# Kernel optimization log

Measured on AMD Instinct MI355X. Metric: run time of the kernel, lower is better.

Reference implementation:

```python
import jax, jax.numpy as jnp
import numpy as np

K = 8
EPS = 1e-5

def knn_idx(x, k):
    # x: (B, C, N) -> idx (B, N, k) nearest neighbors (incl. self)
    xt = jnp.swapaxes(x, 1, 2)  # (B, N, C)
    inner = -2.0 * jnp.einsum('bnc,bmc->bnm', xt, xt)
    xx = jnp.sum(xt * xt, axis=-1)  # (B, N)
    neg_dist = -xx[:, :, None] - inner - xx[:, None, :]
    return jax.lax.top_k(neg_dist, k)[1]

def graph_feature(x, k):
    # x: (B, C, N) -> (B, 2C, N, k)
    B, C, N = x.shape
    idx = knn_idx(x, k)  # (B, N, k)
    xt = jnp.swapaxes(x, 1, 2)  # (B, N, C)
    nb = xt[jnp.arange(B)[:, None, None], idx]  # (B, N, k, C)
    center = xt[:, :, None, :]
    feat = jnp.concatenate([nb - center, jnp.broadcast_to(center, nb.shape)], axis=-1)
    return jnp.transpose(feat, (0, 3, 1, 2))

def bn2d(h, g, b):
    m = jnp.mean(h, axis=(0, 2, 3), keepdims=True)
    v = jnp.var(h, axis=(0, 2, 3), keepdims=True)
    return g[None, :, None, None] * (h - m) * jax.lax.rsqrt(v + EPS) + b[None, :, None, None]

def bn1d(h, g, b):
    m = jnp.mean(h, axis=(0, 2), keepdims=True)
    v = jnp.var(h, axis=(0, 2), keepdims=True)
    return g[None, :, None] * (h - m) * jax.lax.rsqrt(v + EPS) + b[None, :, None]

def fps_idx(xyz, m):
    # xyz: (B, N, 3) furthest point sampling starting at index 0 -> (B, m) int32
    B, N, _ = xyz.shape
    def body(carry, _):
        dist, last = carry
        lastp = jnp.take_along_axis(xyz, last[:, None, None], axis=1)  # (B,1,3)
        d = jnp.sum((xyz - lastp) ** 2, axis=-1)
        dist = jnp.minimum(dist, d)
        nxt = jnp.argmax(dist, axis=-1).astype(jnp.int32)
        return (dist, nxt), last
    init = (jnp.full((B, N), 1e10, dtype=xyz.dtype), jnp.zeros((B,), jnp.int32))
    _, idxs = jax.lax.scan(body, init, None, length=m)
    return jnp.swapaxes(idxs, 0, 1)  # (B, m)

def fps_downsample(coor, x, m):
    # coor: (B,3,N), x: (B,C,N)
    idx = fps_idx(jnp.swapaxes(coor, 1, 2), m)  # (B, m)
    B = coor.shape[0]
    comb = jnp.concatenate([coor, x], axis=1)  # (B, 3+C, N)
    g = jnp.take_along_axis(comb, idx[:, None, :], axis=2)
    return g[:, :3], g[:, 3:]

def edge_block(h, w, g, b):
    f = graph_feature(h, K)                      # (B, 2C, N, k)
    f = jnp.einsum('oc,bcnk->bonk', w, f)        # 1x1 conv2d, no bias
    f = jax.nn.leaky_relu(bn2d(f, g, b), 0.2)
    return jnp.max(f, axis=-1)                   # (B, O, N)

def setup_inputs() -> dict:
    key = jax.random.key(0)
    ks = jax.random.split(key, 16)
    H = 2048
    c16, c8, c4, c2 = H // 16, H // 8, H // 4, H // 2  # 128,256,512,1024
    O2 = 4096 // 2  # 2048
    def w(k, o, c):
        return jax.random.normal(k, (o, c), jnp.float32) * (1.0 / np.sqrt(c))
    inp = {
        'x': jax.random.normal(ks[0], (8, 3, 2048), jnp.float32),
        'w1': w(ks[1], c16, 6),
        'w2': w(ks[2], c16, c8),
        'w3': w(ks[3], c8, c8),
        'w4': w(ks[4], c4, c4),
        'w5': w(ks[5], O2, c2),
        'rw1': w(ks[6], c16, c16),
        'rw2': w(ks[7], c8, c16),
        'rw3': w(ks[8], c4, c8),
    }
    for i, (nm, ch) in enumerate([('1', c16), ('2', c16), ('3', c8), ('4', c4), ('5', O2)]):
        kk = jax.random.split(ks[9 + i], 2)
        inp['g' + nm] = 1.0 + 0.1 * jax.random.normal(kk[0], (ch,), jnp.float32)
        inp['b' + nm] = 0.1 * jax.random.normal(kk[1], (ch,), jnp.float32)
    return inp

def reference(x, w1, w2, w3, w4, w5, rw1, rw2, rw3, g1, b1, g2, b2, g3, b3, g4, b4, g5, b5):
    coor = x
    x1 = edge_block(x, w1, g1, b1)
    x2 = edge_block(x1, w2, g2, b2) + jnp.einsum('oc,bcn->bon', rw1, x1)
    x3 = edge_block(x2, w3, g3, b3) + jnp.einsum('oc,bcn->bon', rw2, x2)
    x4 = edge_block(x3, w4, g4, b4) + jnp.einsum('oc,bcn->bon', rw3, x3)
    h = jnp.concatenate([x1, x2, x3, x4], axis=1)  # (B, 1024, N)
    h = jax.nn.leaky_relu(bn1d(jnp.einsum('oc,bcn->bon', w5, h), g5, b5), 0.2)
    for m in (512, 256, 128):
        coor, h = fps_downsample(coor, h, m)
    f = jnp.concatenate([jnp.max(h, axis=-1), jnp.mean(h, axis=-1)], axis=1)  # (B, 4096)
    return coor, f
```

## Files before the change

### kernel.cpp

```cpp
#include <hip/hip_runtime.h>
#include <float.h>

#define NPTS 2048
#define NB 8
#define KNN 8

typedef short bf16x8 __attribute__((ext_vector_type(8)));
typedef float f32x4  __attribute__((ext_vector_type(4)));

__device__ __forceinline__ float leakyf(float x){ return x > 0.f ? x : 0.2f*x; }

__device__ __forceinline__ unsigned short f2bf(float f){
    unsigned u = __float_as_uint(f);
    return (unsigned short)((u + 0x7FFF + ((u>>16)&1)) >> 16);
}

#define BET(v1,i1,v2,i2) (((v1)>(v2)) || ((v1)==(v2) && (i1)<(i2)))

__device__ __forceinline__ void ins8(float tv[8], int tix[8], float v, int ci)
{
    if (BET(v,ci,tv[7],tix[7])){
        tv[7]=v; tix[7]=ci;
#pragma unroll
        for (int q=7;q>=1;q--){
            if (BET(tv[q],tix[q],tv[q-1],tix[q-1])){
                float t=tv[q]; tv[q]=tv[q-1]; tv[q-1]=t;
                int ti=tix[q]; tix[q]=tix[q-1]; tix[q-1]=ti;
            }
        }
    }
}

__device__ __forceinline__ void merge_write8(float tv[8], int tix[8], int lane,
                                             int* __restrict__ dst)
{
#pragma unroll
    for (int r=0;r<8;r++){
        float bv = tv[0]; int bi = tix[0];
#pragma unroll
        for (int off=32; off; off>>=1){
            float ov = __shfl_xor(bv, off); int oi = __shfl_xor(bi, off);
            if (BET(ov,oi,bv,bi)){ bv=ov; bi=oi; }
        }
        if (tv[0]==bv && tix[0]==bi){
#pragma unroll
            for (int q=0;q<7;q++){ tv[q]=tv[q+1]; tix[q]=tix[q+1]; }
            tv[7]=-FLT_MAX; tix[7]=0x7fffffff;
        }
        if (lane==0) dst[r] = bi;
    }
}

__global__ void transpose_x(const float* __restrict__ x, float* __restrict__ xt)
{
    int g = blockIdx.x*256 + threadIdx.x;
    if (g >= NB*NPTS) return;
    int b = g >> 11, n = g & 2047;
    const float* xb = x + (long)b*3*NPTS;
    xt[g*3+0] = xb[n];
    xt[g*3+1] = xb[NPTS+n];
    xt[g*3+2] = xb[2*NPTS+n];
}

__device__ __forceinline__ unsigned long long u64max(unsigned long long a,
                                                     unsigned long long b)
{ return a > b ? a : b; }

template<int CTRL>
__device__ __forceinline__ unsigned long long dpp_max_step(unsigned long long v)
{
    unsigned plo = (unsigned)__builtin_amdgcn_update_dpp(0, (int)(unsigned)v,      CTRL, 0xF, 0xF, true);
    unsigned phi = (unsigned)__builtin_amdgcn_update_dpp(0, (int)(unsigned)(v>>32), CTRL, 0xF, 0xF, true);
    unsigned long long p = ((unsigned long long)phi << 32) | plo;
    return u64max(v, p);
}

__device__ __forceinline__ unsigned long long wave_reduce_max(unsigned long long v)
{
    v = dpp_max_step<0x111>(v);
    v = dpp_max_step<0x112>(v);
    v = dpp_max_step<0x114>(v);
    v = dpp_max_step<0x118>(v);
    v = dpp_max_step<0x142>(v);
    v = dpp_max_step<0x143>(v);
    return v;
}

template<int NPP>
__device__ void fps_stage_mw(const float4* __restrict__ pts, int m, int* sel,
                             int tid, unsigned long long* wv)
{
    float cx[NPP], cy[NPP], cz[NPP], dist[NPP];
#pragma unroll
    for (int r=0;r<NPP;r++){
        float4 p = pts[r*256 + tid];
        cx[r]=p.x; cy[r]=p.y; cz[r]=p.z; dist[r]=1e10f;
    }
    int w = tid>>6, lane = tid&63;
    int last = 0;
    if (tid==0) sel[0]=0;
    for (int i=1;i<m;i++){
        float4 lp = pts[last];
#pragma unroll
        for (int r=0;r<NPP;r++){
            float dx=__fsub_rn(cx[r],lp.x), dy=__fsub_rn(cy[r],lp.y), dz=__fsub_rn(cz[r],lp.z);
            float d = __fadd_rn(__fadd_rn(__fmul_rn(dx,dx), __fmul_rn(dy,dy)), __fmul_rn(dz,dz));
            dist[r] = fminf(dist[r], d);
        }
        unsigned long long t[(NPP+1)/2];
        if (NPP == 1){
            t[0] = ((unsigned long long)__float_as_uint(dist[0])<<32) | (unsigned)(2047 - tid);
        } else {
#pragma unroll
            for (int k=0;k<NPP/2;k++){
                unsigned long long a = ((unsigned long long)__float_as_uint(dist[2*k  ])<<32) | (unsigned)(2047 - ((2*k  )*256+tid));
                unsigned long long b = ((unsigned long long)__float_as_uint(dist[2*k+1])<<32) | (unsigned)(2047 - ((2*k+1)*256+tid));
                t[k] = u64max(a, b);
            }
#pragma unroll
            for (int s=NPP/4; s>=1; s>>=1)
#pragma unroll
                for (int k=0;k<s;k++) t[k] = u64max(t[k], t[k+s]);
        }
        unsigned long long best = wave_reduce_max(t[0]);
        if (lane==63) wv[(i&1)*4 + w] = best;
        __syncthreads();
        unsigned long long b0 = wv[(i&1)*4+0], b1 = wv[(i&1)*4+1];
        unsigned long long b2 = wv[(i&1)*4+2], b3 = wv[(i&1)*4+3];
        best = u64max(u64max(b0,b1), u64max(b2,b3));
        int win = 2047 - (int)(unsigned)best;
        last = win;
        if (tid==0) sel[i] = win;
    }
}

struct FpsSh {
    float4 pts1[2048]; float4 pts2[512]; float4 pts3[256];
    int sel1[512]; int sel2[256]; int sel3[128];
    unsigned long long wv[8];
};
struct GemmSh { __align__(16) float As[16][132]; __align__(16) float Bs[16][132]; };
union ShU { FpsSh f; GemmSh g; };

__device__ void fps_block(const float* __restrict__ x, int* __restrict__ idxF,
                          float* __restrict__ coorOut, int b, int tid, FpsSh& sh)
{
    const float* xb = x + (long)b*3*NPTS;
    for (int i=tid;i<2048;i+=256)
        sh.pts1[i] = make_float4(xb[i], xb[NPTS+i], xb[2*NPTS+i], 0.f);
    __syncthreads();
    fps_stage_mw<8>(sh.pts1, 512, sh.sel1, tid, sh.wv);
    __syncthreads();
    for (int i=tid;i<512;i+=256) sh.pts2[i] = sh.pts1[sh.sel1[i]];
    __syncthreads();
    fps_stage_mw<2>(sh.pts2, 256, sh.sel2, tid, sh.wv);
    __syncthreads();
    for (int i=tid;i<256;i+=256) sh.pts3[i] = sh.pts2[sh.sel2[i]];
    __syncthreads();
    fps_stage_mw<1>(sh.pts3, 128, sh.sel3, tid, sh.wv);
    __syncthreads();
    for (int i=tid;i<128;i+=256){
        int gi = sh.sel1[sh.sel2[sh.sel3[i]]];
        idxF[b*128+i] = gi;
        float4 p = sh.pts1[gi];
        coorOut[(long)b*384 + 0*128 + i] = p.x;
        coorOut[(long)b*384 + 1*128 + i] = p.y;
        coorOut[(long)b*384 + 2*128 + i] = p.z;
    }
}

__global__ __launch_bounds__(256)
void knn_c3(const float* __restrict__ x, int* __restrict__ idx)
{
    __shared__ float sx[NPTS], sy[NPTS], sz[NPTS];
    int b = blockIdx.x >> 7, rblk = blockIdx.x & 127;
    const float* xb = x + (long)b*3*NPTS;
    int tid = threadIdx.x;
    for (int i=tid;i<NPTS;i+=256){
        sx[i]=xb[i]; sy[i]=xb[NPTS+i]; sz[i]=xb[2*NPTS+i];
    }
    __syncthreads();
    int w = tid>>6, lane = tid&63;
    for (int rr=0; rr<4; rr++){
        int n = rblk*16 + w*4 + rr;
        float px=sx[n], py=sy[n], pz=sz[n];
        float tv[8]; int tix[8];
#pragma unroll
        for (int i=0;i<8;i++){ tv[i]=-FLT_MAX; tix[i]=0x7fffffff; }
        for (int it=0; it<8; it++){
            int c = it*256 + lane*4;
            float4 qx = *(const float4*)&sx[c];
            float4 qy = *(const float4*)&sy[c];
            float4 qz = *(const float4*)&sz[c];
            float dx, dy, dz;
            dx=qx.x-px; dy=qy.x-py; dz=qz.x-pz;
            ins8(tv,tix, -fmaf(dx,dx,fmaf(dy,dy,dz*dz)), c+0);
            dx=qx.y-px; dy=qy.y-py; dz=qz.y-pz;
            ins8(tv,tix, -fmaf(dx,dx,fmaf(dy,dy,dz*dz)), c+1);
            dx=qx.z-px; dy=qy.z-py; dz=qz.z-pz;
            ins8(tv,tix, -fmaf(dx,dx,fmaf(dy,dy,dz*dz)), c+2);
            dx=qx.w-px; dy=qy.w-py; dz=qz.w-pz;
            ins8(tv,tix, -fmaf(dx,dx,fmaf(dy,dy,dz*dz)), c+3);
        }
        merge_write8(tv, tix, lane, idx + ((long)(b*NPTS+n))*KNN);
    }
}

__global__ void prep_w(const float* __restrict__ w, const float* __restrict__ rw,
                       float* __restrict__ wcat, int O, int C, int hasR)
{
    int t = blockIdx.x*256 + threadIdx.x;
    if (t >= O*C) return;
    int o = t / C, c = t % C;
    float a = w[o*2*C + c];
    wcat[o*C + c] = a;
    wcat[(O+o)*C + c] = w[o*2*C + C + c] - a;
    if (hasR) wcat[(2*O+o)*C + c] = rw[o*C + c];
}

__global__ void rownorm(const float* __restrict__ X, float* __restrict__ xx,
                        int lda, int C)
{
    int g = blockIdx.x*256 + threadIdx.x;
    if (g >= NB*NPTS) return;
    const float* r = X + (long)g*lda;
    float s = 0.f;
    for (int c=0;c<C;c++) s += r[c]*r[c];
    xx[g] = s;
}

template<int VEC, bool SYM>
__device__ __forceinline__ void gemm_body(
    float (*As)[132], float (*Bs)[132],
    const float* __restrict__ A, const float* __restrict__ B, float* __restrict__ C,
    int Kd, int lda, int ldb, int ldc, int bx, int by, int tid)
{
    int tm = by * 128, tn = bx * 128;
    int ty = tid >> 4, tx = tid & 15;
    int cn0 = tx*4, cn1 = 64 + tx*4;
    float acc[8][8] = {};
    for (int k0 = 0; k0 < Kd; k0 += 16){
        if (VEC == 4){
#pragma unroll
            for (int i=0;i<2;i++){
                int e = tid + i*256;
                int rr = e >> 2, kq = e & 3;
                float4 av = *(const float4*)(A + (long)(tm+rr)*lda + k0 + kq*4);
                float4 bv = *(const float4*)(B + (long)(tn+rr)*ldb + k0 + kq*4);
                As[kq*4+0][rr]=av.x; As[kq*4+1][rr]=av.y; As[kq*4+2][rr]=av.z; As[kq*4+3][rr]=av.w;
                Bs[kq*4+0][rr]=bv.x; Bs[kq*4+1][rr]=bv.y; Bs[kq*4+2][rr]=bv.z; Bs[kq*4+3][rr]=bv.w;
            }
        } else {
#pragma unroll
            for (int i=0;i<8;i++){
                int e = tid + i*256;
                int kk = e & 15, rr = e >> 4;
                int ak = k0 + kk;
                As[kk][rr] = (ak < Kd) ? A[(long)(tm+rr)*lda + ak] : 0.f;
                Bs[kk][rr] = (ak < Kd) ? B[(long)(tn+rr)*ldb + ak] : 0.f;
            }
        }
        __syncthreads();
#pragma unroll
        for (int kk=0;kk<16;kk++){
            float4 a01 = *(const float4*)&As[kk][ty*8];
            float4 a23 = *(const float4*)&As[kk][ty*8+4];
            float4 b01 = *(const float4*)&Bs[kk][cn0];
            float4 b23 = *(const float4*)&Bs[kk][cn1];
            float aa[8] = {a01.x,a01.y,a01.z,a01.w,a23.x,a23.y,a23.z,a23.w};
            float bb[8] = {b01.x,b01.y,b01.z,b01.w,b23.x,b23.y,b23.z,b23.w};
#pragma unroll
            for (int i=0;i<8;i++)
#pragma unroll
                for (int j=0;j<8;j++)
                    acc[i][j] += aa[i]*bb[j];
        }
        __syncthreads();
    }
#pragma unroll
    for (int i=0;i<8;i++){
        long r = tm + ty*8 + i;
        float4 v0 = {acc[i][0],acc[i][1],acc[i][2],acc[i][3]};
        float4 v1 = {acc[i][4],acc[i][5],acc[i][6],acc[i][7]};
        *(float4*)(C + r*ldc + tn + cn0) = v0;
        *(float4*)(C + r*ldc + tn + cn1) = v1;
    }
    if (SYM && bx != by){
#pragma unroll
        for (int j=0;j<4;j++){
            long r0 = tn + cn0 + j;
            long r1 = tn + cn1 + j;
            float4 u0 = {acc[0][j],  acc[1][j],  acc[2][j],  acc[3][j]};
            float4 u1 = {acc[4][j],  acc[5][j],  acc[6][j],  acc[7][j]};
            float4 u2 = {acc[0][j+4],acc[1][j+4],acc[2][j+4],acc[3][j+4]};
            float4 u3 = {acc[4][j+4],acc[5][j+4],acc[6][j+4],acc[7][j+4]};
            *(float4*)(C + r0*ldc + tm + ty*8)     = u0;
            *(float4*)(C + r0*ldc + tm + ty*8 + 4) = u1;
            *(float4*)(C + r1*ldc + tm + ty*8)     = u2;
            *(float4*)(C + r1*ldc + tm + ty*8 + 4) = u3;
        }
    }
}

template<int VEC, bool SYM>
__global__ __launch_bounds__(256)
void gemm_nt(const float* __restrict__ A, const float* __restrict__ B,
             float* __restrict__ C,
             int Kd, int lda, int ldb, int ldc,
             long sA, long sB, long sC)
{
    if (SYM && blockIdx.y > blockIdx.x) return;
    __shared__ GemmSh sh;
    int bz = blockIdx.z;
    gemm_body<VEC,SYM>(sh.As, sh.Bs, A + (long)bz*sA, B + (long)bz*sB,
                       C + (long)bz*sC, Kd, lda, ldb, ldc,
                       blockIdx.x, blockIdx.y, threadIdx.x);
}

__global__ __launch_bounds__(256)
void uvr_fps(const float* __restrict__ A, const float* __restrict__ B,
             float* __restrict__ C, int Kd, int lda, int ldb, int ldc, int nx,
             const float* __restrict__ x, int* __restrict__ idxF,
             float* __restrict__ coorOut)
{
    __shared__ ShU sh;
    if (blockIdx.x < 8){
        fps_block(x, idxF, coorOut, blockIdx.x, threadIdx.x, sh.f);
        return;
    }
    int id = blockIdx.x - 8;
    gemm_body<4,false>(sh.g.As, sh.g.Bs, A, B, C, Kd, lda, ldb, ldc,
                       id % nx, id / nx, threadIdx.x);
}

__global__ __launch_bounds__(256)
void topk8(const float* __restrict__ D, const float* __restrict__ xx,
           int* __restrict__ idx, int b0)
{
    int tid = threadIdx.x, w = tid>>6, lane = tid & 63;
    int gr = blockIdx.x*4 + w;
    int b = b0 + (gr >> 11);
    const float* drow = D + (long)gr*NPTS;
    const float* xb = xx + (long)b*NPTS;
    float tv[8]; int tix[8];
#pragma unroll
    for (int i=0;i<8;i++){ tv[i]=-FLT_MAX; tix[i]=0x7fffffff; }
    for (int it=0; it<8; it++){
        int c = it*256 + lane*4;
        float4 d4 = *(const float4*)(drow + c);
        float4 x4 = *(const float4*)(xb + c);
        ins8(tv,tix, 2.f*d4.x - x4.x, c+0);
        ins8(tv,tix, 2.f*d4.y - x4.y, c+1);
        ins8(tv,tix, 2.f*d4.z - x4.z, c+2);
        ins8(tv,tix, 2.f*d4.w - x4.w, c+3);
    }
    merge_write8(tv, tix, lane, idx + ((long)(b0*NPTS) + gr)*KNN);
}

__global__ __launch_bounds__(256)
void stats_edge(const float* __restrict__ uvr, const int* __restrict__ idx,
                float* __restrict__ ps, float* __restrict__ pq,
                float* __restrict__ mxb, float* __restrict__ mnb,
                int O, int ld)
{
    int tid = threadIdx.x;
    int r0 = blockIdx.x * 128;
    float s0=0,q0=0,s1=0,q1=0;
    for (int rr=0; rr<128; rr++){
        int g = r0 + rr;
        int b = g >> 11;
        const int* ip = idx + (long)g*KNN;
        const float* vrow = uvr + (long)g*ld + O;
        const float* ub[8];
#pragma unroll
        for (int k=0;k<8;k++) ub[k] = uvr + (long)((b<<11) + ip[k])*ld;
        int o = tid;
        if (o < O){
            float vv = vrow[o];
            float mx=-FLT_MAX, mn=FLT_MAX;
#pragma unroll
            for (int k=0;k<8;k++){
                float f = ub[k][o]+vv;
                s0+=f; q0+=f*f; mx=fmaxf(mx,f); mn=fminf(mn,f);
            }
            mxb[(long)g*O+o]=mx; mnb[(long)g*O+o]=mn;
        }
        o = tid + 256;
        if (o < O){
            float vv = vrow[o];
            float mx=-FLT_MAX, mn=FLT_MAX;
#pragma unroll
            for (int k=0;k<8;k++){
                float f = ub[k][o]+vv;
                s1+=f; q1+=f*f; mx=fmaxf(mx,f); mn=fminf(mn,f);
            }
            mxb[(long)g*O+o]=mx; mnb[(long)g*O+o]=mn;
        }
    }
    if (tid < O){ ps[blockIdx.x*2048 + tid] = s0; pq[blockIdx.x*2048 + tid] = q0; }
    if (tid+256 < O){ ps[blockIdx.x*2048 + tid+256] = s1; pq[blockIdx.x*2048 + tid+256] = q1; }
}

__global__ void reduce_stats(const float* __restrict__ ps, const float* __restrict__ pq,
                             const float* __restrict__ gam, const float* __restrict__ bet,
                             float* __restrict__ ab, float* __restrict__ cb,
                             int O, int np, float invCnt)
{
    int o = blockIdx.x*256 + threadIdx.x;
    if (o >= O) return;
    float s=0.f, q=0.f;
    for (int p=0;p<np;p++){ s += ps[p*2048 + o]; q += pq[p*2048 + o]; }
    float m = s * invCnt;
    float var = q * invCnt - m*m;
    float a = gam[o] * rsqrtf(var + 1e-5f);
    ab[o] = a;
    cb[o] = bet[o] - m*a;
}

__global__ void finalize_edge(const float* __restrict__ mxb, const float* __restrict__ mnb,
                              const float* __restrict__ uvr,
                              const float* __restrict__ ab, const float* __restrict__ cb,
                              float* __restrict__ hcat, int lgO, int ld, int hoff, int hasR)
{
    long t = (long)blockIdx.x*256 + threadIdx.x;
    int O = 1 << lgO;
    int o = (int)(t & (O-1));
    int g = (int)(t >> lgO);
    float a = ab[o], c = cb[o];
    float mx = mxb[t], mn = mnb[t];
    float zz = (a > 0.f) ? (a*mx + c) : (a*mn + c);
    float outv = leakyf(zz);
    if (hasR) outv += uvr[(long)g*ld + 2*O + o];
    hcat[(long)g*1024 + hoff + o] = outv;
}

__global__ void colsum_fin(const float* __restrict__ part, float* __restrict__ hbar)
{
    int tid = threadIdx.x;
    float4 acc = {0,0,0,0};
    for (int p=0;p<128;p++){
        float4 v = ((const float4*)part)[p*256 + tid];
        acc.x+=v.x; acc.y+=v.y; acc.z+=v.z; acc.w+=v.w;
    }
    ((float4*)hbar)[tid] = acc;
}

__global__ __launch_bounds__(256)
void gram_colsum(const float* __restrict__ H, float* __restrict__ P,
                 float* __restrict__ cspart)
{
    __shared__ __align__(16) unsigned short As[128][40];
    __shared__ __align__(16) unsigned short Bs[128][40];
    int tid = threadIdx.x;
    if (blockIdx.x >= 288){
        int pb = blockIdx.x - 288;
        const float4* h4 = (const float4*)(H + (long)pb*128*1024);
        float4 acc = {0,0,0,0};
        for (int r=0;r<128;r++){
            float4 v = h4[r*256 + tid];
            acc.x+=v.x; acc.y+=v.y; acc.z+=v.z; acc.w+=v.w;
        }
        ((float4*)cspart)[pb*256 + tid] = acc;
        return;
    }
    int bz = blockIdx.x / 36, t36 = blockIdx.x % 36;
    int I = 0, q = t36, accq = 8;
    while (q >= accq){ q -= accq; accq--; I++; }
    int ti = (I + q)*128, tj = I*128;
    int w = tid>>6, lane = tid&63;
    int wr = (w>>1)*64, wc = (w&1)*64;
    f32x4 acc[16];
#pragma unroll
    for (int i=0;i<16;i++) acc[i] = (f32x4){0.f,0.f,0.f,0.f};
    const float* Hc = H + (long)bz*2048*1024;
    for (int m0=0; m0<2048; m0+=32){
#pragma unroll
        for (int it=0; it<4; it++){
            int e = tid + it*256;
            int mm = e >> 5;
            int c4 = (e & 31) * 4;
            const float* row = Hc + (long)(m0+mm)*1024;
            float4 av = *(const float4*)(row + ti + c4);
            float4 bv = *(const float4*)(row + tj + c4);
            int mg = mm >> 3, ml = mm & 7;
            float fa[4] = {av.x, av.y, av.z, av.w};
            float fb[4] = {bv.x, bv.y, bv.z, bv.w};
#pragma unroll
            for (int qq=0; qq<4; qq++){
                int ia = c4 + qq;
                int pos = ((mg ^ ((ia>>2)&3))<<3) + ml;
                As[ia][pos] = f2bf(fa[qq]);
                Bs[ia][pos] = f2bf(fb[qq]);
            }
        }
        __syncthreads();
        bf16x8 af[4], bf[4];
#pragma unroll
        for (int f=0; f<4; f++){
            int ra = wr + f*16 + (lane&15);
            int ga = ((lane>>4) ^ ((ra>>2)&3)) << 3;
            af[f] = *(const bf16x8*)&As[ra][ga];
            int rb = wc + f*16 + (lane&15);
            int gb = ((lane>>4) ^ ((rb>>2)&3)) << 3;
            bf[f] = *(const bf16x8*)&Bs[rb][gb];
        }
#pragma unroll
        for (int fi=0; fi<4; fi++)
#pragma unroll
        for (int fj=0; fj<4; fj++)
            acc[fi*4+fj] = __builtin_amdgcn_mfma_f32_16x16x32_bf16(
                af[fi], bf[fj], acc[fi*4+fj], 0, 0, 0);
        __syncthreads();
    }
    float* Pp = P + ((long)bz<<20);
#pragma unroll
    for (int fi=0; fi<4; fi++)
#pragma unroll
    for (int fj=0; fj<4; fj++){
        int row0 = ti + wr + fi*16 + (lane>>4)*4;
        int col  = tj + wc + fj*16 + (lane&15);
#pragma unroll
        for (int r4=0; r4<4; r4++)
            Pp[(long)(row0+r4)*1024 + col] = acc[fi*4+fj][r4];
    }
}

__global__ void greduce(const float* __restrict__ P, float* __restrict__ G)
{
    long i4 = (long)blockIdx.x*256 + threadIdx.x;
    float4 a = ((const float4*)P)[i4];
    for (int p=1;p<8;p++){
        float4 v = ((const float4*)P)[((long)p<<18) + i4];
        a.x+=v.x; a.y+=v.y; a.z+=v.z; a.w+=v.w;
    }
    ((float4*)G)[i4] = a;
}

__global__ void mirror_g(float* __restrict__ G)
{
    __shared__ float t[64][65];
    int q = blockIdx.x, I = 0, acc = 15;
    while (q >= acc){ q -= acc; acc--; I++; }
    int J = I + 1 + q;
    int tid = threadIdx.x;
#pragma unroll
    for (int k=0;k<16;k++){
        int e = tid + k*256;
        int sr = e>>6, sc = e&63;
        t[sr][sc] = G[(long)(J*64+sr)*1024 + I*64+sc];
    }
    __syncthreads();
#pragma unroll
    for (int k=0;k<16;k++){
        int e = tid + k*256;
        int dr = e>>6, dc = e&63;
        G[(long)(I*64+dr)*1024 + J*64+dc] = t[dc][dr];
    }
}

__global__ void bn5_prep(const float* __restrict__ w5, const float* __restrict__ T,
                         const float* __restrict__ hbar,
                         const float* __restrict__ g5, const float* __restrict__ b5,
                         float* __restrict__ ab, float* __restrict__ cb)
{
    int w = threadIdx.x>>6, lane = threadIdx.x&63;
    int n = blockIdx.x*4 + w;
    const float4* wr = (const float4*)(w5 + (long)n*1024);
    const float4* tr = (const float4*)(T  + (long)n*1024);
    const float4* hb = (const float4*)hbar;
    float s1=0.f, s2=0.f;
    for (int i=lane;i<256;i+=64){
        float4 wv = wr[i], t4 = tr[i], hv = hb[i];
        s1 += wv.x*hv.x + wv.y*hv.y + wv.z*hv.z + wv.w*hv.w;
        s2 += wv.x*t4.x + wv.y*t4.y + wv.z*t4.z + wv.w*t4.w;
    }
#pragma unroll
    for (int off=32; off; off>>=1){
        s1 += __shfl_xor(s1, off);
        s2 += __shfl_xor(s2, off);
    }
    if (lane==0){
        float m = s1*(1.f/16384.f);
        float qq = s2*(1.f/16384.f);
        float var = qq - m*m;
        float a = g5[n]*rsqrtf(var+1e-5f);
        ab[n]=a; cb[n]=b5[n]-m*a;
    }
}

__global__ void gather_rows(const float* __restrict__ src, const int* __restrict__ idxF,
                            float* __restrict__ dst)
{
    int r = blockIdx.x;
    int b = r >> 7;
    int srow = (b<<11) + idxF[r];
    const float4* s = (const float4*)(src + (long)srow*1024);
    float4* d = (float4*)(dst + (long)r*1024);
    for (int c=threadIdx.x; c<256; c+=256) d[c] = s[c];
}

__global__ void finalize_f(const float* __restrict__ zsel, const float* __restrict__ ab,
                           const float* __restrict__ cb, float* __restrict__ out)
{
    int b = blockIdx.x >> 3, oc = blockIdx.x & 7;
    int o = oc*256 + threadIdx.x;
    float a = ab[o], c = cb[o];
    float mx = -FLT_MAX, sm = 0.f;
    const float* zp = zsel + (long)b*128*2048 + o;
    for (int i=0;i<128;i++){
        float v = leakyf(a*zp[(long)i*2048] + c);
        mx = fmaxf(mx, v); sm += v;
    }
    out[b*4096 + o] = mx;
    out[b*4096 + 2048 + o] = sm * (1.f/128.f);
}

extern "C" void kernel_launch(void* const* d_in, const int* in_sizes, int n_in,
                              void* d_out, int out_size, void* d_ws, size_t ws_size,
                              hipStream_t stream)
{
    (void)in_sizes; (void)n_in; (void)out_size; (void)ws_size;
    const float* x   = (const float*)d_in[0];
    const float* w1  = (const float*)d_in[1];
    const float* w2  = (const float*)d_in[2];
    const float* w3  = (const float*)d_in[3];
    const float* w4  = (const float*)d_in[4];
    const float* w5  = (const float*)d_in[5];
    const float* rw1 = (const float*)d_in[6];
    const float* rw2 = (const float*)d_in[7];
    const float* rw3 = (const float*)d_in[8];
    const float* g1  = (const float*)d_in[9];  const float* b1 = (const float*)d_in[10];
    const float* g2  = (const float*)d_in[11]; const float* b2 = (const float*)d_in[12];
    const float* g3  = (const float*)d_in[13]; const float* b3 = (const float*)d_in[14];
    const float* g4  = (const float*)d_in[15]; const float* b4 = (const float*)d_in[16];
    const float* g5  = (const float*)d_in[17]; const float* b5 = (const float*)d_in[18];
    float* out = (float*)d_out;

    char* wsb = (char*)d_ws;
    size_t off = 0;
    auto alloc = [&](size_t bytes)->char* {
        char* p = wsb + off;
        off += (bytes + 255) & ~(size_t)255;
        return p;
    };
    float* xt    = (float*)alloc((size_t)16384*3*4);
    float* hcat  = (float*)alloc((size_t)16384*1024*4);
    float* uvr   = (float*)alloc((size_t)16384*1536*4);
    float* Dbuf  = uvr;
    float* gramP = uvr;
    float* G     = (float*)alloc((size_t)1024*1024*4);
    float* T     = (float*)alloc((size_t)2048*1024*4);
    float* zselA = (float*)alloc((size_t)1024*1024*4);
    float* zsel  = (float*)alloc((size_t)1024*2048*4);
    float* mxb   = (float*)alloc((size_t)16384*512*4);
    float* mnb   = (float*)alloc((size_t)16384*512*4);
    float* xx    = (float*)alloc((size_t)16384*4);
    int*   idx   = (int*)  alloc((size_t)16384*8*4);
    float* wcat  = (float*)alloc((size_t)1536*256*4);
    float* ps    = (float*)alloc((size_t)128*2048*4);
    float* pq    = (float*)alloc((size_t)128*2048*4);
    float* cspart= (float*)alloc((size_t)128*1024*4);
    float* hbar  = (float*)alloc((size_t)1024*4);
    float* ab    = (float*)alloc((size_t)2048*4);
    float* cb    = (float*)alloc((size_t)2048*4);
    int*   idxF  = (int*)  alloc((size_t)1024*4);

    transpose_x<<<64, 256, 0, stream>>>(x, xt);

    struct EB {
        const float* X; int lda, C, O, lgO, hoff, hasR;
        const float* w; const float* rw; const float* g; const float* bb;
    };
    EB eb[4] = {
        { xt,        3,    3,   128, 7, 0,   0, w1, nullptr, g1, b1 },
        { hcat+0,    1024, 128, 128, 7, 128, 1, w2, rw1,     g2, b2 },
        { hcat+128,  1024, 128, 256, 8, 256, 1, w3, rw2,     g3, b3 },
        { hcat+256,  1024, 256, 512, 9, 512, 1, w4, rw3,     g4, b4 },
    };
    for (int i=0;i<4;i++){
        EB e = eb[i];
        int ld = (2 + e.hasR) * e.O;
        int nx = ld / 128;
        int tot = e.O * e.C;
        prep_w<<<(tot+255)/256, 256, 0, stream>>>(e.w, e.rw, wcat, e.O, e.C, e.hasR);
        if (i == 0){
            knn_c3<<<1024, 256, 0, stream>>>(x, idx);
            gemm_nt<1,false><<<dim3(nx, 128, 1), 256, 0, stream>>>(
                e.X, wcat, uvr, e.C, e.lda, e.C, ld, 0, 0, 0);
        } else {
            rownorm<<<64, 256, 0, stream>>>(e.X, xx, e.lda, e.C);
            for (int b0=0; b0<8; b0+=4){
                const float* Ab = e.X + (long)b0*NPTS*e.lda;
                gemm_nt<4,true><<<dim3(16,16,4), 256, 0, stream>>>(
                    Ab, Ab, Dbuf, e.C, e.lda, e.lda, 2048,
                    (long)NPTS*e.lda, (long)NPTS*e.lda, (long)NPTS*NPTS);
                topk8<<<2048, 256, 0, stream>>>(Dbuf, xx, idx, b0);
            }
            if (i == 3)
                uvr_fps<<<8 + nx*128, 256, 0, stream>>>(
                    e.X, wcat, uvr, e.C, e.lda, e.C, ld, nx, x, idxF, out);
            else
                gemm_nt<4,false><<<dim3(nx, 128, 1), 256, 0, stream>>>(
                    e.X, wcat, uvr, e.C, e.lda, e.C, ld, 0, 0, 0);
        }
        stats_edge<<<128, 256, 0, stream>>>(uvr, idx, ps, pq, mxb, mnb, e.O, ld);
        reduce_stats<<<(e.O+255)/256, 256, 0, stream>>>(ps, pq, e.g, e.bb, ab, cb,
                                                        e.O, 128, 1.f/131072.f);
        finalize_edge<<<64*e.O, 256, 0, stream>>>(mxb, mnb, uvr, ab, cb, hcat,
                                                  e.lgO, ld, e.hoff, e.hasR);
    }

    gram_colsum<<<288 + 128, 256, 0, stream>>>(hcat, gramP, cspart);
    colsum_fin<<<1, 256, 0, stream>>>(cspart, hbar);
    greduce<<<1024, 256, 0, stream>>>(gramP, G);
    mirror_g<<<120, 256, 0, stream>>>(G);
    gemm_nt<4,false><<<dim3(8,16,1), 256, 0, stream>>>(
        w5, G, T, 1024, 1024, 1024, 1024, 0, 0, 0);
    bn5_prep<<<512, 256, 0, stream>>>(w5, T, hbar, g5, b5, ab, cb);
    gather_rows<<<1024, 256, 0, stream>>>(hcat, idxF, zselA);
    gemm_nt<4,false><<<dim3(16,8,1), 256, 0, stream>>>(
        zselA, w5, zsel, 1024, 1024, 1024, 2048, 0, 0, 0);
    finalize_f<<<64, 256, 0, stream>>>(zsel, ab, cb, out + 3072);
}
```

Baseline: 3.052 ms.

## Merge kNN Gram and edge GEMM into one launch; split-K small tail GEMMs

For edge blocks 2-4, a single launch now runs the symmetric Gram GEMM for the first four batches alongside the edge-feature GEMM (and FPS for the last block). This fills the GPU better and removes one serialized launch. Dbuf grows to hold four batches and is reused for the mxb/mnb buffers. The two late 1024-K GEMMs (w5·G and zsel) are split four ways along K into partial buffers that bn5_prep and finalize_f sum, which exposes more blocks on small grids at the cost of extra partial-sum traffic and tighter buffer aliasing.

```diff
diff --git a/kernel.cpp b/kernel.cpp
--- a/kernel.cpp
+++ b/kernel.cpp
@@ -141,6 +141,11 @@
 };
 struct GemmSh { __align__(16) float As[16][132]; __align__(16) float Bs[16][132]; };
 union ShU { FpsSh f; GemmSh g; };
+
+template<bool B> struct ShPick { using T = GemmSh; };
+template<> struct ShPick<true> { using T = ShU; };
+__device__ __forceinline__ GemmSh& gemsh(GemmSh& s){ return s; }
+__device__ __forceinline__ GemmSh& gemsh(ShU& u){ return u.g; }
 
 __device__ void fps_block(const float* __restrict__ x, int* __restrict__ idxF,
                           float* __restrict__ coorOut, int b, int tid, FpsSh& sh)
@@ -317,20 +322,32 @@
                        blockIdx.x, blockIdx.y, threadIdx.x);
 }
 
+template<bool FPS>
 __global__ __launch_bounds__(256)
-void uvr_fps(const float* __restrict__ A, const float* __restrict__ B,
-             float* __restrict__ C, int Kd, int lda, int ldb, int ldc, int nx,
-             const float* __restrict__ x, int* __restrict__ idxF,
-             float* __restrict__ coorOut)
-{
-    __shared__ ShU sh;
-    if (blockIdx.x < 8){
-        fps_block(x, idxF, coorOut, blockIdx.x, threadIdx.x, sh.f);
+void edge_mega(const float* __restrict__ X, const float* __restrict__ W,
+               float* __restrict__ D, float* __restrict__ U,
+               int Kd, int lda, int ld, int nxU,
+               const float* __restrict__ x, int* __restrict__ idxF,
+               float* __restrict__ coorOut)
+{
+    __shared__ typename ShPick<FPS>::T sh;
+    int id = blockIdx.x;
+    if constexpr (FPS){
+        if (id < 8){ fps_block(x, idxF, coorOut, id, threadIdx.x, ((ShU&)sh).f); return; }
+        id -= 8;
+    }
+    GemmSh& g = gemsh(sh);
+    if (id < 1024){
+        int bz = id >> 8, r = id & 255, by = r >> 4, bx = r & 15;
+        if (by > bx) return;
+        const float* Xz = X + (long)bz*NPTS*lda;
+        gemm_body<4,true>(g.As, g.Bs, Xz, Xz, D + (long)bz*NPTS*NPTS,
+                          Kd, lda, lda, 2048, bx, by, threadIdx.x);
         return;
     }
-    int id = blockIdx.x - 8;
-    gemm_body<4,false>(sh.g.As, sh.g.Bs, A, B, C, Kd, lda, ldb, ldc,
-                       id % nx, id / nx, threadIdx.x);
+    id -= 1024;
+    gemm_body<4,false>(g.As, g.Bs, X, W, U, Kd, lda, Kd, ld,
+                       id % nxU, id / nxU, threadIdx.x);
 }
 
 __global__ __launch_bounds__(256)
@@ -566,11 +583,17 @@
     int w = threadIdx.x>>6, lane = threadIdx.x&63;
     int n = blockIdx.x*4 + w;
     const float4* wr = (const float4*)(w5 + (long)n*1024);
-    const float4* tr = (const float4*)(T  + (long)n*1024);
+    const float4* t0 = (const float4*)(T + (long)n*1024);
+    const float4* t1 = (const float4*)(T + (1L<<21) + (long)n*1024);
+    const float4* t2 = (const float4*)(T + (2L<<21) + (long)n*1024);
+    const float4* t3 = (const float4*)(T + (3L<<21) + (long)n*1024);
     const float4* hb = (const float4*)hbar;
     float s1=0.f, s2=0.f;
     for (int i=lane;i<256;i+=64){
-        float4 wv = wr[i], t4 = tr[i], hv = hb[i];
+        float4 wv = wr[i], hv = hb[i];
+        float4 a0=t0[i], a1=t1[i], a2=t2[i], a3=t3[i];
+        float4 t4 = {a0.x+a1.x+a2.x+a3.x, a0.y+a1.y+a2.y+a3.y,
+                     a0.z+a1.z+a2.z+a3.z, a0.w+a1.w+a2.w+a3.w};
         s1 += wv.x*hv.x + wv.y*hv.y + wv.z*hv.z + wv.w*hv.w;
         s2 += wv.x*t4.x + wv.y*t4.y + wv.z*t4.z + wv.w*t4.w;
     }
@@ -607,8 +630,11 @@
     float a = ab[o], c = cb[o];
     float mx = -FLT_MAX, sm = 0.f;
     const float* zp = zsel + (long)b*128*2048 + o;
+    const long PS = (long)1024*2048;
     for (int i=0;i<128;i++){
-        float v = leakyf(a*zp[(long)i*2048] + c);
+        long ofs = (long)i*2048;
+        float z = zp[ofs] + zp[PS+ofs] + zp[2*PS+ofs] + zp[3*PS+ofs];
+        float v = leakyf(a*z + c);
         mx = fmaxf(mx, v); sm += v;
     }
     out[b*4096 + o] = mx;
@@ -646,14 +672,14 @@
     float* xt    = (float*)alloc((size_t)16384*3*4);
     float* hcat  = (float*)alloc((size_t)16384*1024*4);
     float* uvr   = (float*)alloc((size_t)16384*1536*4);
-    float* Dbuf  = uvr;
     float* gramP = uvr;
+    float* T     = uvr;
+    float* zsel  = uvr + (size_t)8*1024*1024;
+    float* Dbuf  = (float*)alloc((size_t)4*2048*2048*4);
+    float* mxb   = Dbuf;
+    float* mnb   = Dbuf + (size_t)16384*512;
     float* G     = (float*)alloc((size_t)1024*1024*4);
-    float* T     = (float*)alloc((size_t)2048*1024*4);
     float* zselA = (float*)alloc((size_t)1024*1024*4);
-    float* zsel  = (float*)alloc((size_t)1024*2048*4);
-    float* mxb   = (float*)alloc((size_t)16384*512*4);
-    float* mnb   = (float*)alloc((size_t)16384*512*4);
     float* xx    = (float*)alloc((size_t)16384*4);
     int*   idx   = (int*)  alloc((size_t)16384*8*4);
     float* wcat  = (float*)alloc((size_t)1536*256*4);
@@ -680,28 +706,28 @@
     for (int i=0;i<4;i++){
         EB e = eb[i];
         int ld = (2 + e.hasR) * e.O;
-        int nx = ld / 128;
+        int nxU = ld / 128;
         int tot = e.O * e.C;
         prep_w<<<(tot+255)/256, 256, 0, stream>>>(e.w, e.rw, wcat, e.O, e.C, e.hasR);
         if (i == 0){
             knn_c3<<<1024, 256, 0, stream>>>(x, idx);
-            gemm_nt<1,false><<<dim3(nx, 128, 1), 256, 0, stream>>>(
+            gemm_nt<1,false><<<dim3(nxU, 128, 1), 256, 0, stream>>>(
                 e.X, wcat, uvr, e.C, e.lda, e.C, ld, 0, 0, 0);
         } else {
             rownorm<<<64, 256, 0, stream>>>(e.X, xx, e.lda, e.C);
-            for (int b0=0; b0<8; b0+=4){
-                const float* Ab = e.X + (long)b0*NPTS*e.lda;
-                gemm_nt<4,true><<<dim3(16,16,4), 256, 0, stream>>>(
-                    Ab, Ab, Dbuf, e.C, e.lda, e.lda, 2048,
-                    (long)NPTS*e.lda, (long)NPTS*e.lda, (long)NPTS*NPTS);
-                topk8<<<2048, 256, 0, stream>>>(Dbuf, xx, idx, b0);
-            }
             if (i == 3)
-                uvr_fps<<<8 + nx*128, 256, 0, stream>>>(
-                    e.X, wcat, uvr, e.C, e.lda, e.C, ld, nx, x, idxF, out);
+                edge_mega<true><<<8 + 1024 + nxU*128, 256, 0, stream>>>(
+                    e.X, wcat, Dbuf, uvr, e.C, e.lda, ld, nxU, x, idxF, out);
             else
-                gemm_nt<4,false><<<dim3(nx, 128, 1), 256, 0, stream>>>(
-                    e.X, wcat, uvr, e.C, e.lda, e.C, ld, 0, 0, 0);
+                edge_mega<false><<<1024 + nxU*128, 256, 0, stream>>>(
+                    e.X, wcat, Dbuf, uvr, e.C, e.lda, ld, nxU,
+                    nullptr, nullptr, nullptr);
+            topk8<<<2048, 256, 0, stream>>>(Dbuf, xx, idx, 0);
+            const float* X4 = e.X + (long)4*NPTS*e.lda;
+            gemm_nt<4,true><<<dim3(16,16,4), 256, 0, stream>>>(
+                X4, X4, Dbuf, e.C, e.lda, e.lda, 2048,
+                (long)NPTS*e.lda, (long)NPTS*e.lda, (long)NPTS*NPTS);
+            topk8<<<2048, 256, 0, stream>>>(Dbuf, xx, idx, 4);
         }
         stats_edge<<<128, 256, 0, stream>>>(uvr, idx, ps, pq, mxb, mnb, e.O, ld);
         reduce_stats<<<(e.O+255)/256, 256, 0, stream>>>(ps, pq, e.g, e.bb, ab, cb,
@@ -714,11 +740,11 @@
     colsum_fin<<<1, 256, 0, stream>>>(cspart, hbar);
     greduce<<<1024, 256, 0, stream>>>(gramP, G);
     mirror_g<<<120, 256, 0, stream>>>(G);
-    gemm_nt<4,false><<<dim3(8,16,1), 256, 0, stream>>>(
-        w5, G, T, 1024, 1024, 1024, 1024, 0, 0, 0);
+    gemm_nt<4,false><<<dim3(8,16,4), 256, 0, stream>>>(
+        w5, G, T, 256, 1024, 1024, 1024, 256, 256, (long)2048*1024);
     bn5_prep<<<512, 256, 0, stream>>>(w5, T, hbar, g5, b5, ab, cb);
     gather_rows<<<1024, 256, 0, stream>>>(hcat, idxF, zselA);
-    gemm_nt<4,false><<<dim3(16,8,1), 256, 0, stream>>>(
-        zselA, w5, zsel, 1024, 1024, 1024, 2048, 0, 0, 0);
+    gemm_nt<4,false><<<dim3(16,8,4), 256, 0, stream>>>(
+        zselA, w5, zsel, 256, 1024, 1024, 2048, 256, 256, (long)1024*2048);
     finalize_f<<<64, 256, 0, stream>>>(zsel, ab, cb, out + 3072);
 }
```

Result: faster. 2.826 ms (-7.4%).
